# Optimization experiments

Measured on AMD Instinct MI355X. Metric: run time of the kernel, lower is better.

The kernel has to match this reference:

```python
import jax, jax.numpy as jnp
import numpy as np

B, N, D = 8, 1024, 1024

def setup_inputs() -> dict:
    key = jax.random.key(0)
    k1, k2, k3, k4, k5 = jax.random.split(key, 5)
    x = jax.random.normal(k1, (B, N, D), dtype=jnp.float32)
    y = jax.random.normal(k2, (B, N, D), dtype=jnp.float32)
    adj = jax.random.uniform(k3, (B, N, N), dtype=jnp.float32)
    adj_sumrow = jnp.sum(adj, axis=-1, keepdims=True)  # [B, N, 1], row-sum normalizer
    W = jax.random.normal(k4, (D, D), dtype=jnp.float32) * (1.0 / np.sqrt(D))
    b = jax.random.normal(k5, (D,), dtype=jnp.float32) * 0.02
    return {"x": x, "y": y, "adj": adj, "adj_sumrow": adj_sumrow, "W": W, "b": b}

def reference(x, y, adj, adj_sumrow, W, b):
    # GraphConvolutionCustom: project neighbor features, aggregate via dense adj,
    # normalize by row-sum, add bias and residual input x; then ReLU.
    # Dropout is identity in eval mode (training=False).
    support = jnp.einsum('bnd,de->bne', y, W)          # [B, N, D]
    agg = jnp.matmul(adj, support) / adj_sumrow        # [B, N, D]
    out = jax.nn.relu(agg + b + x)
    return out
```

## Files before the change

kernel.cpp:

```cpp
#include <hip/hip_runtime.h>
#include <hip/hip_bf16.h>
#include <stdint.h>


typedef float  f32x4  __attribute__((ext_vector_type(4)));
typedef __bf16 bf16x8 __attribute__((ext_vector_type(8)));

__device__ __forceinline__ unsigned short f2bf(float f) {
  union { float f; unsigned int u; } c; c.f = f;
  unsigned int u = c.u;
  u += 0x7FFFu + ((u >> 16) & 1u);
  return (unsigned short)(u >> 16);
}

__device__ __forceinline__ void async_cp16(const void* g, void* l) {
  __builtin_amdgcn_global_load_lds(
      (const __attribute__((address_space(1))) unsigned int*)g,
      (__attribute__((address_space(3))) unsigned int*)l, 16, 0, 0);
}

__device__ __forceinline__ void bar() { asm volatile("s_barrier" ::: "memory"); }

__device__ __forceinline__ void zero_acc(f32x4 acc[4][4]) {
#pragma unroll
  for (int i = 0; i < 4; ++i)
#pragma unroll
    for (int j = 0; j < 4; ++j)
#pragma unroll
      for (int r = 0; r < 4; ++r) acc[i][j][r] = 0.0f;
}


__global__ __launch_bounds__(256) void k_prep(
    const float4* __restrict__ y4, const float4* __restrict__ a4,
    ushort4* __restrict__ yb, ushort4* __restrict__ ab,
    const float* __restrict__ W, unsigned short* __restrict__ Wt)
{
  __shared__ float t[64][65];
  const int bid = blockIdx.x;
  if (bid < 16384) {
    const int i = bid * 256 + threadIdx.x;
    const bool isY = i < 2097152;
    const float4 v = isY ? y4[i] : a4[i - 2097152];
    ushort4 p;
    p.x = f2bf(v.x); p.y = f2bf(v.y); p.z = f2bf(v.z); p.w = f2bf(v.w);
    if (isY) yb[i] = p; else ab[i - 2097152] = p;
  } else {
    const int id = bid - 16384;
    const int n0 = (id & 15) * 64, k0 = (id >> 4) * 64;
    const int tx = threadIdx.x & 63, ty = threadIdx.x >> 6;
#pragma unroll
    for (int r = ty; r < 64; r += 4)
      t[r][tx] = W[(size_t)(k0 + r) * 1024 + n0 + tx];
    __syncthreads();
#pragma unroll
    for (int r = ty; r < 64; r += 4)
      Wt[(size_t)(n0 + r) * 1024 + k0 + tx] = f2bf(t[tx][r]);
  }
}


__device__ __forceinline__ void gemm_pipe(
    const unsigned short* __restrict__ A,  int sA,
    const unsigned short* __restrict__ Bt, int sB,
    int m0, int n0, f32x4 acc[4][4], unsigned short* lsm, int tid)
{
  const int lane = tid & 63, wave = tid >> 6;
  const int wm = (wave >> 1) * 64, wn = (wave & 1) * 64;
  const int quad = lane >> 4, l16 = lane & 15;
  const int rg   = lane >> 2;
  const int colo = (((lane & 3) - rg) & 3) * 8;

  auto issue_stage = [&](int s) {
    const int k0 = s << 5;
    unsigned short* ls = lsm + (s & 3) * 8192;
#pragma unroll
    for (int t = 0; t < 2; ++t) {
      const int g = wave * 2 + t;
      async_cp16(A  + (size_t)(m0 + g * 16 + rg) * sA + k0 + colo, ls + g * 512);
      async_cp16(Bt + (size_t)(n0 + g * 16 + rg) * sB + k0 + colo, ls + 4096 + g * 512);
    }
  };

  issue_stage(0); issue_stage(1); issue_stage(2);

#pragma unroll 1
  for (int s = 0; s < 32; ++s) {
    if (s < 29) {
      issue_stage(s + 3);
      asm volatile("s_waitcnt vmcnt(12)" ::: "memory");
    } else if (s == 29) { asm volatile("s_waitcnt vmcnt(8)" ::: "memory");
    } else if (s == 30) { asm volatile("s_waitcnt vmcnt(4)" ::: "memory");
    } else              { asm volatile("s_waitcnt vmcnt(0)" ::: "memory"); }
    bar();

    const unsigned short* ls = lsm + (s & 3) * 8192;
    bf16x8 af[4], bfr[4];
#pragma unroll
    for (int i = 0; i < 4; ++i) {
      const int r = wm + i * 16 + l16;
      af[i]  = *(const bf16x8*)(ls + r * 32 + ((quad + r) & 3) * 8);
    }
#pragma unroll
    for (int j = 0; j < 4; ++j) {
      const int r = wn + j * 16 + l16;
      bfr[j] = *(const bf16x8*)(ls + 4096 + r * 32 + ((quad + r) & 3) * 8);
    }
#pragma unroll
    for (int i = 0; i < 4; ++i)
#pragma unroll
      for (int j = 0; j < 4; ++j)
        acc[i][j] = __builtin_amdgcn_mfma_f32_16x16x32_bf16(af[i], bfr[j], acc[i][j], 0, 0, 0);

    asm volatile("s_waitcnt lgkmcnt(0)" ::: "memory");
    bar();
  }
}


__global__ __launch_bounds__(256) void k_gemm1(
    const unsigned short* __restrict__ Wt,
    const unsigned short* __restrict__ Ybf,
    unsigned short* __restrict__ Sup2)
{
  __shared__ __align__(16) unsigned short lsm[4 * 8192];
  const int tid = threadIdx.x;
  const int n0 = blockIdx.x * 128, m0 = blockIdx.y * 128;

  f32x4 acc[4][4];
  zero_acc(acc);
  gemm_pipe(Wt, 1024, Ybf, 1024, m0, n0, acc, lsm, tid);

  const int lane = tid & 63, wave = tid >> 6;
  const int wm = (wave >> 1) * 64, wn = (wave & 1) * 64;
  const int quad = lane >> 4, l16 = lane & 15;
#pragma unroll
  for (int i = 0; i < 4; ++i) {
    const int mb = m0 + wm + i * 16 + quad * 4;
#pragma unroll
    for (int r = 0; r < 4; ++r) {
      unsigned short* row = Sup2 + ((size_t)(mb + r) << 13);
#pragma unroll
      for (int j = 0; j < 4; ++j)
        row[n0 + wn + j * 16 + l16] = f2bf(acc[i][j][r]);
    }
  }
}


__global__ __launch_bounds__(256) void k_gemm2(
    const unsigned short* __restrict__ AdjBf,
    const unsigned short* __restrict__ Sup2,
    const float* __restrict__ x,
    const float* __restrict__ sumrow,
    const float* __restrict__ bias,
    float* __restrict__ out)
{
  __shared__ __align__(16) unsigned short lsm[4 * 8192];
  const int tid = threadIdx.x;
  const int n0 = blockIdx.x * 128, m0 = blockIdx.y * 128, b = blockIdx.z;

  f32x4 acc[4][4];
  zero_acc(acc);
  gemm_pipe(AdjBf + ((size_t)b << 20), 1024,
            Sup2 + ((size_t)b << 10), 8192,
            m0, n0, acc, lsm, tid);

  const float* xb = x   + ((size_t)b << 20);
  float*       ob = out + ((size_t)b << 20);
  const float* sr = sumrow + ((size_t)b << 10);
  const int lane = tid & 63, wave = tid >> 6;
  const int wm = (wave >> 1) * 64, wn = (wave & 1) * 64;
  const int quad = lane >> 4, l16 = lane & 15;

  float bv[4];
#pragma unroll
  for (int j = 0; j < 4; ++j) bv[j] = bias[n0 + wn + j * 16 + l16];

#pragma unroll
  for (int i = 0; i < 4; ++i) {
    const int mb = m0 + wm + i * 16 + quad * 4;
#pragma unroll
    for (int r = 0; r < 4; ++r) {
      const int m = mb + r;
      const float inv = 1.0f / sr[m];
#pragma unroll
      for (int j = 0; j < 4; ++j) {
        const int n = n0 + wn + j * 16 + l16;
        const size_t idx = (((size_t)m) << 10) + n;
        float v = acc[i][j][r] * inv + bv[j] + xb[idx];
        ob[idx] = fmaxf(v, 0.0f);
      }
    }
  }
}


extern "C" void kernel_launch(void* const* d_in, const int* in_sizes, int n_in,
                              void* d_out, int out_size, void* d_ws, size_t ws_size,
                              hipStream_t stream) {
  const float* x      = (const float*)d_in[0];
  const float* y      = (const float*)d_in[1];
  const float* adj    = (const float*)d_in[2];
  const float* sumrow = (const float*)d_in[3];
  const float* W      = (const float*)d_in[4];
  const float* bias   = (const float*)d_in[5];
  float* out = (float*)d_out;

  char* ws = (char*)d_ws;
  unsigned short* ybf   = (unsigned short*)(ws);
  unsigned short* adjbf = (unsigned short*)(ws + ((size_t)16 << 20));
  unsigned short* wt    = (unsigned short*)(ws + ((size_t)32 << 20));
  unsigned short* sup2  = (unsigned short*)(ws + ((size_t)34 << 20));

  k_prep<<<dim3(16640), dim3(256), 0, stream>>>(
      (const float4*)y, (const float4*)adj, (ushort4*)ybf, (ushort4*)adjbf, W, wt);
  k_gemm1<<<dim3(64, 8), dim3(256), 0, stream>>>(wt, ybf, sup2);
  k_gemm2<<<dim3(8, 8, 8), dim3(256), 0, stream>>>(adjbf, sup2, x, sumrow, bias, out);
}
```

Measured before the change: 204.9 us.

## Fuse fp32-to-bf16 conversion of y and adj into GEMM tile loads

Drops the standalone conversion pass that wrote bf16 copies of y and adj to workspace. Both GEMMs now read fp32 tiles straight into registers, convert them to bf16, and store them swizzled into LDS, while the bf16 operand is still loaded asynchronously. The software pipeline and vmcnt accounting are reorganized around the mixed register/async loads. This removes a full read-write round trip of 64 MB of activations, but doubles the global bytes read per GEMM tile for the fp32 operand and adds conversion ALU work inside the main loop.

```diff
diff --git a/kernel.cpp b/kernel.cpp
--- a/kernel.cpp
+++ b/kernel.cpp
@@ -1,16 +1,15 @@
 #include <hip/hip_runtime.h>
-#include <hip/hip_bf16.h>
 #include <stdint.h>
 
 
 typedef float  f32x4  __attribute__((ext_vector_type(4)));
 typedef __bf16 bf16x8 __attribute__((ext_vector_type(8)));
 
-__device__ __forceinline__ unsigned short f2bf(float f) {
+__device__ __forceinline__ unsigned int f2bf(float f) {
   union { float f; unsigned int u; } c; c.f = f;
   unsigned int u = c.u;
   u += 0x7FFFu + ((u >> 16) & 1u);
-  return (unsigned short)(u >> 16);
+  return u >> 16;
 }
 
 __device__ __forceinline__ void async_cp16(const void* g, void* l) {
@@ -19,7 +18,9 @@
       (__attribute__((address_space(3))) unsigned int*)l, 16, 0, 0);
 }
 
-__device__ __forceinline__ void bar() { asm volatile("s_barrier" ::: "memory"); }
+__device__ __forceinline__ void lgkbar() {
+  asm volatile("s_waitcnt lgkmcnt(0)\n\ts_barrier" ::: "memory");
+}
 
 __device__ __forceinline__ void zero_acc(f32x4 acc[4][4]) {
 #pragma unroll
@@ -31,96 +32,122 @@
 }
 
 
-__global__ __launch_bounds__(256) void k_prep(
-    const float4* __restrict__ y4, const float4* __restrict__ a4,
-    ushort4* __restrict__ yb, ushort4* __restrict__ ab,
+__global__ __launch_bounds__(256) void k_prepW(
     const float* __restrict__ W, unsigned short* __restrict__ Wt)
 {
   __shared__ float t[64][65];
-  const int bid = blockIdx.x;
-  if (bid < 16384) {
-    const int i = bid * 256 + threadIdx.x;
-    const bool isY = i < 2097152;
-    const float4 v = isY ? y4[i] : a4[i - 2097152];
-    ushort4 p;
-    p.x = f2bf(v.x); p.y = f2bf(v.y); p.z = f2bf(v.z); p.w = f2bf(v.w);
-    if (isY) yb[i] = p; else ab[i - 2097152] = p;
-  } else {
-    const int id = bid - 16384;
-    const int n0 = (id & 15) * 64, k0 = (id >> 4) * 64;
-    const int tx = threadIdx.x & 63, ty = threadIdx.x >> 6;
-#pragma unroll
-    for (int r = ty; r < 64; r += 4)
-      t[r][tx] = W[(size_t)(k0 + r) * 1024 + n0 + tx];
-    __syncthreads();
-#pragma unroll
-    for (int r = ty; r < 64; r += 4)
-      Wt[(size_t)(n0 + r) * 1024 + k0 + tx] = f2bf(t[tx][r]);
-  }
-}
-
-
-__device__ __forceinline__ void gemm_pipe(
-    const unsigned short* __restrict__ A,  int sA,
-    const unsigned short* __restrict__ Bt, int sB,
-    int m0, int n0, f32x4 acc[4][4], unsigned short* lsm, int tid)
+  const int tx = threadIdx.x, ty = threadIdx.y;
+  const int n0 = blockIdx.x * 64, k0 = blockIdx.y * 64;
+#pragma unroll
+  for (int r = ty; r < 64; r += 4)
+    t[r][tx] = W[(size_t)(k0 + r) * 1024 + n0 + tx];
+  __syncthreads();
+#pragma unroll
+  for (int r = ty; r < 64; r += 4)
+    Wt[(size_t)(n0 + r) * 1024 + k0 + tx] = (unsigned short)f2bf(t[tx][r]);
+}
+
+
+__device__ __forceinline__ void gemm_core(
+    const unsigned short* __restrict__ G, int sG, int g0,
+    const float* __restrict__ F, int sF, int f0,
+    int moff, int noff,
+    f32x4 acc[4][4], unsigned short* lsm, int tid)
 {
   const int lane = tid & 63, wave = tid >> 6;
   const int wm = (wave >> 1) * 64, wn = (wave & 1) * 64;
   const int quad = lane >> 4, l16 = lane & 15;
-  const int rg   = lane >> 2;
-  const int colo = (((lane & 3) - rg) & 3) * 8;
-
-  auto issue_stage = [&](int s) {
-    const int k0 = s << 5;
-    unsigned short* ls = lsm + (s & 3) * 8192;
+  const int fc = ((quad + (l16 >> 1)) & 3) * 8;
+  const int gr = lane >> 2;
+  const int gq = (((lane & 3) - ((lane >> 3) & 7)) & 3) * 8;
+  const int fr = tid >> 3;
+  const int fcol = (tid & 7) * 4;
+  const int wq = (tid & 7) >> 1;
+  const int whalf = (tid & 1) * 4;
+
+  auto issueG = [&](int s) {
+    unsigned short* st = lsm + (s & 3) * 8192;
 #pragma unroll
     for (int t = 0; t < 2; ++t) {
       const int g = wave * 2 + t;
-      async_cp16(A  + (size_t)(m0 + g * 16 + rg) * sA + k0 + colo, ls + g * 512);
-      async_cp16(Bt + (size_t)(n0 + g * 16 + rg) * sB + k0 + colo, ls + 4096 + g * 512);
-    }
-  };
-
-  issue_stage(0); issue_stage(1); issue_stage(2);
+      async_cp16(G + (size_t)(g0 + g * 16 + gr) * sG + s * 32 + gq, st + g * 512);
+    }
+  };
+  auto loadF = [&](int s, float4* slot) {
+#pragma unroll
+    for (int j = 0; j < 4; ++j)
+      slot[j] = *(const float4*)(F + (size_t)(f0 + j * 32 + fr) * sF + s * 32 + fcol);
+  };
+  auto writeF = [&](int s, const float4* slot) {
+    unsigned short* st = lsm + (s & 3) * 8192 + 4096;
+#pragma unroll
+    for (int j = 0; j < 4; ++j) {
+      const int r = j * 32 + fr;
+      const int p = (wq + ((r & 15) >> 1)) & 3;
+      uint2 v;
+      v.x = f2bf(slot[j].x) | (f2bf(slot[j].y) << 16);
+      v.y = f2bf(slot[j].z) | (f2bf(slot[j].w) << 16);
+      *(uint2*)(st + r * 32 + p * 8 + whalf) = v;
+    }
+  };
+  auto compute = [&](int s) {
+    const unsigned short* st = lsm + (s & 3) * 8192;
+    bf16x8 mf[4], nf[4];
+#pragma unroll
+    for (int i = 0; i < 4; ++i)
+      mf[i] = *(const bf16x8*)(st + moff + (wm + i * 16 + l16) * 32 + fc);
+#pragma unroll
+    for (int j = 0; j < 4; ++j)
+      nf[j] = *(const bf16x8*)(st + noff + (wn + j * 16 + l16) * 32 + fc);
+#pragma unroll
+    for (int i = 0; i < 4; ++i)
+#pragma unroll
+      for (int j = 0; j < 4; ++j)
+        acc[i][j] = __builtin_amdgcn_mfma_f32_16x16x32_bf16(mf[i], nf[j], acc[i][j], 0, 0, 0);
+  };
+
+  float4 s0[4], s1[4], t0[4], t1[4];
+  loadF(0, t0);
+  loadF(1, t1);
+  issueG(0); issueG(1);
+  loadF(2, s0);
+  issueG(2);
+  loadF(3, s1);
+  asm volatile("s_waitcnt vmcnt(18)" ::: "memory");
+  writeF(0, t0);
+  asm volatile("s_waitcnt vmcnt(14)" ::: "memory");
+  writeF(1, t1);
+  lgkbar();
+
+  auto body = [&](int s, float4* slot, int K1, bool doG, bool doW, bool doRB, bool fin) {
+    if (doG) issueG(s + 3);
+    if (doW) {
+      if (K1 == 8)      asm volatile("s_waitcnt vmcnt(8)" ::: "memory");
+      else if (K1 == 2) asm volatile("s_waitcnt vmcnt(2)" ::: "memory");
+      writeF(s + 2, slot);
+    }
+    if (doRB) loadF(s + 4, slot);
+    if (fin) asm volatile("s_waitcnt vmcnt(0)" ::: "memory");
+    lgkbar();
+    compute(s);
+    lgkbar();
+  };
 
 #pragma unroll 1
-  for (int s = 0; s < 32; ++s) {
-    if (s < 29) {
-      issue_stage(s + 3);
-      asm volatile("s_waitcnt vmcnt(12)" ::: "memory");
-    } else if (s == 29) { asm volatile("s_waitcnt vmcnt(8)" ::: "memory");
-    } else if (s == 30) { asm volatile("s_waitcnt vmcnt(4)" ::: "memory");
-    } else              { asm volatile("s_waitcnt vmcnt(0)" ::: "memory"); }
-    bar();
-
-    const unsigned short* ls = lsm + (s & 3) * 8192;
-    bf16x8 af[4], bfr[4];
-#pragma unroll
-    for (int i = 0; i < 4; ++i) {
-      const int r = wm + i * 16 + l16;
-      af[i]  = *(const bf16x8*)(ls + r * 32 + ((quad + r) & 3) * 8);
-    }
-#pragma unroll
-    for (int j = 0; j < 4; ++j) {
-      const int r = wn + j * 16 + l16;
-      bfr[j] = *(const bf16x8*)(ls + 4096 + r * 32 + ((quad + r) & 3) * 8);
-    }
-#pragma unroll
-    for (int i = 0; i < 4; ++i)
-#pragma unroll
-      for (int j = 0; j < 4; ++j)
-        acc[i][j] = __builtin_amdgcn_mfma_f32_16x16x32_bf16(af[i], bfr[j], acc[i][j], 0, 0, 0);
-
-    asm volatile("s_waitcnt lgkmcnt(0)" ::: "memory");
-    bar();
+  for (int ss = 0; ss < 28; ss += 2) {
+    body(ss,     s0, 8, true, true, true, false);
+    body(ss + 1, s1, 8, true, true, true, false);
   }
+  body(28, s0, 8, true,  true,  false, false);
+  body(29, s1, 2, false, true,  false, false);
+  body(30, s0, 0, false, false, false, false);
+  body(31, s0, 0, false, false, false, true);
 }
 
 
 __global__ __launch_bounds__(256) void k_gemm1(
     const unsigned short* __restrict__ Wt,
-    const unsigned short* __restrict__ Ybf,
+    const float* __restrict__ Y,
     unsigned short* __restrict__ Sup2)
 {
   __shared__ __align__(16) unsigned short lsm[4 * 8192];
@@ -129,7 +156,7 @@
 
   f32x4 acc[4][4];
   zero_acc(acc);
-  gemm_pipe(Wt, 1024, Ybf, 1024, m0, n0, acc, lsm, tid);
+  gemm_core(Wt, 1024, m0, Y, 1024, n0, 0, 4096, acc, lsm, tid);
 
   const int lane = tid & 63, wave = tid >> 6;
   const int wm = (wave >> 1) * 64, wn = (wave & 1) * 64;
@@ -142,14 +169,14 @@
       unsigned short* row = Sup2 + ((size_t)(mb + r) << 13);
 #pragma unroll
       for (int j = 0; j < 4; ++j)
-        row[n0 + wn + j * 16 + l16] = f2bf(acc[i][j][r]);
+        row[n0 + wn + j * 16 + l16] = (unsigned short)f2bf(acc[i][j][r]);
     }
   }
 }
 
 
 __global__ __launch_bounds__(256) void k_gemm2(
-    const unsigned short* __restrict__ AdjBf,
+    const float* __restrict__ Adj,
     const unsigned short* __restrict__ Sup2,
     const float* __restrict__ x,
     const float* __restrict__ sumrow,
@@ -162,9 +189,9 @@
 
   f32x4 acc[4][4];
   zero_acc(acc);
-  gemm_pipe(AdjBf + ((size_t)b << 20), 1024,
-            Sup2 + ((size_t)b << 10), 8192,
-            m0, n0, acc, lsm, tid);
+  gemm_core(Sup2 + ((size_t)b << 10), 8192, n0,
+            Adj + ((size_t)b << 20), 1024, m0,
+            4096, 0, acc, lsm, tid);
 
   const float* xb = x   + ((size_t)b << 20);
   float*       ob = out + ((size_t)b << 20);
@@ -208,13 +235,10 @@
   float* out = (float*)d_out;
 
   char* ws = (char*)d_ws;
-  unsigned short* ybf   = (unsigned short*)(ws);
-  unsigned short* adjbf = (unsigned short*)(ws + ((size_t)16 << 20));
-  unsigned short* wt    = (unsigned short*)(ws + ((size_t)32 << 20));
-  unsigned short* sup2  = (unsigned short*)(ws + ((size_t)34 << 20));
-
-  k_prep<<<dim3(16640), dim3(256), 0, stream>>>(
-      (const float4*)y, (const float4*)adj, (ushort4*)ybf, (ushort4*)adjbf, W, wt);
-  k_gemm1<<<dim3(64, 8), dim3(256), 0, stream>>>(wt, ybf, sup2);
-  k_gemm2<<<dim3(8, 8, 8), dim3(256), 0, stream>>>(adjbf, sup2, x, sumrow, bias, out);
-}
+  unsigned short* wt   = (unsigned short*)(ws);
+  unsigned short* sup2 = (unsigned short*)(ws + ((size_t)2 << 20));
+
+  k_prepW<<<dim3(16, 16), dim3(64, 4), 0, stream>>>(W, wt);
+  k_gemm1<<<dim3(64, 8), dim3(256), 0, stream>>>(wt, y, sup2);
+  k_gemm2<<<dim3(8, 8, 8), dim3(256), 0, stream>>>(adj, sup2, x, sumrow, bias, out);
+}
```

Result: slower. 212.0 us (+3.4%).
